# Kernel tuning notes

Measured on AMD Instinct MI355X. Metric: run time of the kernel, lower is better.

The kernel has to match this reference:

```python
import jax, jax.numpy as jnp
import numpy as np

B, S, SE, D, V, L, H = 32, 256, 1024, 512, 8000, 4, 8
EPS = 1e-3   # keras BatchNormalization default epsilon
NEG = -1e9


def _heads(x, W, b):
    Bx, Sx, Dx = x.shape
    return (jnp.einsum('bsd,de->bse', x, W) + b).reshape(Bx, Sx, H, Dx // H).transpose(0, 2, 1, 3)


def mha(q_in, kv_in, Wq, bq, Wk, bk, Wv, bv, Wo, bo, causal):
    dk = q_in.shape[-1] // H
    q = _heads(q_in, Wq, bq)   # [B,H,Sq,dk]
    k = _heads(kv_in, Wk, bk)  # [B,H,Sk,dk]
    v = _heads(kv_in, Wv, bv)
    scores = jnp.einsum('bhqd,bhkd->bhqk', q, k) / jnp.sqrt(jnp.asarray(dk, q.dtype))
    if causal:
        # original loop uses values = x[:, :j, :] -> token j attends to STRICTLY previous tokens;
        # token 0 has zero keys, so its attention output is exactly zero (before Wo bias).
        Sq, Sk = scores.shape[-2], scores.shape[-1]
        mask = jnp.arange(Sk)[None, :] < jnp.arange(Sq)[:, None]
        attn = jax.nn.softmax(jnp.where(mask, scores, NEG), axis=-1)
        attn = jnp.where(mask, attn, 0.0)
    else:
        attn = jax.nn.softmax(scores, axis=-1)
    out = jnp.einsum('bhqk,bhkd->bhqd', attn, v)
    out = out.transpose(0, 2, 1, 3).reshape(q_in.shape[0], q_in.shape[1], -1)
    return out @ Wo + bo


def bn(x, gamma, beta, mean, var):
    # keras BatchNorm, inference mode, axis=-1
    return gamma * (x - mean) * jax.lax.rsqrt(var + EPS) + beta


def setup_inputs():
    key = jax.random.key(0)
    ks = iter(jax.random.split(key, 80))

    def rn(*shape):
        return jax.random.normal(next(ks), shape, jnp.float32) * 0.02

    inp = {
        'sequence': jax.random.randint(next(ks), (B, S), 0, V, jnp.int32),
        'encoder_output': jax.random.normal(next(ks), (B, SE, D), jnp.float32),
        'pos_encodings': jax.random.normal(next(ks), (S, D), jnp.float32),
        'emb': rn(V, D),
        'Wout': rn(D, V), 'bout': jnp.zeros((V,), jnp.float32),
        'W1': rn(L, D, 512), 'b1': jnp.zeros((L, 512), jnp.float32),
        'W2': rn(L, 512, D), 'b2': jnp.zeros((L, D), jnp.float32),
    }
    for p in ('bot', 'mid'):
        for nm in ('Wq', 'Wk', 'Wv', 'Wo'):
            inp[f'{nm}_{p}'] = rn(L, D, D)
        for nm in ('bq', 'bk', 'bv', 'bo'):
            inp[f'{nm}_{p}'] = jnp.zeros((L, D), jnp.float32)
    for p in ('bot', 'mid', 'ffn'):
        inp[f'gamma_{p}'] = jnp.ones((L, D), jnp.float32)
        inp[f'beta_{p}'] = jnp.zeros((L, D), jnp.float32)
        inp[f'mean_{p}'] = jnp.zeros((L, D), jnp.float32)
        inp[f'var_{p}'] = jnp.ones((L, D), jnp.float32)
    return inp


def reference(sequence, encoder_output, pos_encodings, emb, Wout, bout, W1, b1, W2, b2,
              Wq_bot, Wk_bot, Wv_bot, Wo_bot, bq_bot, bk_bot, bv_bot, bo_bot,
              Wq_mid, Wk_mid, Wv_mid, Wo_mid, bq_mid, bk_mid, bv_mid, bo_mid,
              gamma_bot, beta_bot, mean_bot, var_bot,
              gamma_mid, beta_mid, mean_mid, var_mid,
              gamma_ffn, beta_ffn, mean_ffn, var_ffn):
    x = emb[sequence] + pos_encodings[None, :, :]  # [B,S,D]
    for i in range(L):
        a = mha(x, x, Wq_bot[i], bq_bot[i], Wk_bot[i], bk_bot[i], Wv_bot[i], bv_bot[i], Wo_bot[i], bo_bot[i], True)
        x = bn(x + a, gamma_bot[i], beta_bot[i], mean_bot[i], var_bot[i])
        a = mha(x, encoder_output, Wq_mid[i], bq_mid[i], Wk_mid[i], bk_mid[i], Wv_mid[i], bv_mid[i], Wo_mid[i], bo_mid[i], False)
        x = bn(x + a, gamma_mid[i], beta_mid[i], mean_mid[i], var_mid[i])
        f = jax.nn.relu(x @ W1[i] + b1[i]) @ W2[i] + b2[i]
        x = bn(x + f, gamma_ffn[i], beta_ffn[i], mean_ffn[i], var_ffn[i])
    return x @ Wout + bout  # logits [B,S,V]
```

## Files before the change

### kernel.cpp

```cpp
#include <hip/hip_runtime.h>
#include <hip/hip_fp16.h>

typedef _Float16 half8 __attribute__((ext_vector_type(8)));
typedef _Float16 half4 __attribute__((ext_vector_type(4)));
typedef float floatx4 __attribute__((ext_vector_type(4)));

#define NB 32
#define NS 256
#define NSE 1024
#define ND 512
#define NV 8000
#define NVP 8064
#define NL 4
#define NH 8
#define NDK 64
#define BN_EPS 1e-3f

typedef const __attribute__((address_space(1))) void* gas_ptr;
typedef __attribute__((address_space(3))) void* las_ptr;
__device__ __forceinline__ void gload16(const void* g, void* l) {
    __builtin_amdgcn_global_load_lds((gas_ptr)g, (las_ptr)l, 16, 0, 0);
}

__global__ __launch_bounds__(256) void k_cast(const float* __restrict__ in, _Float16* __restrict__ out) {
    size_t i = ((size_t)blockIdx.x * 256 + threadIdx.x) * 8;
    float4 a = *(const float4*)(in + i);
    float4 b = *(const float4*)(in + i + 4);
    half8 o;
    o[0] = (_Float16)a.x; o[1] = (_Float16)a.y; o[2] = (_Float16)a.z; o[3] = (_Float16)a.w;
    o[4] = (_Float16)b.x; o[5] = (_Float16)b.y; o[6] = (_Float16)b.z; o[7] = (_Float16)b.w;
    *(half8*)(out + i) = o;
}

__global__ __launch_bounds__(256) void k_embed(const int* __restrict__ seq,
                                               const float* __restrict__ emb,
                                               const float* __restrict__ pos,
                                               _Float16* __restrict__ x) {
    size_t i = ((size_t)blockIdx.x * 256 + threadIdx.x) * 8;
    int tok = (int)(i / ND);
    int d = (int)(i % ND);
    int s = tok % NS;
    int t = seq[tok];
    const float* ep = emb + (size_t)t * ND + d;
    const float* pp = pos + (size_t)s * ND + d;
    half8 o;
    for (int j = 0; j < 8; j++) o[j] = (_Float16)(ep[j] + pp[j]);
    *(half8*)(x + i) = o;
}

__global__ void k_transpose_w(const float* __restrict__ in, _Float16* __restrict__ out, int R, int C,
                              long long ostride) {
    __shared__ float tile[32][33];
    int b = blockIdx.z;
    int c0 = blockIdx.x * 32, r0 = blockIdx.y * 32;
    const float* pin = in + (size_t)b * R * C;
    _Float16* pout = out + (size_t)b * ostride;
    int tx = threadIdx.x, ty = threadIdx.y;
    for (int j = 0; j < 32; j += 8)
        tile[ty + j][tx] = pin[(size_t)(r0 + ty + j) * C + c0 + tx];
    __syncthreads();
    for (int j = 0; j < 32; j += 8)
        pout[(size_t)(c0 + ty + j) * R + r0 + tx] = (_Float16)tile[tx][ty + j];
}

template<int BM, int BK>
__global__ __launch_bounds__(256) void k_gemm(
    const _Float16* __restrict__ A, const _Float16* __restrict__ Bt,
    const float* __restrict__ bias0, const float* __restrict__ bias1, const float* __restrict__ bias2,
    void* __restrict__ C0, void* __restrict__ C1, void* __restrict__ C2,
    int M, int N, int K, int relu, int mode, int Sb,
    const _Float16* __restrict__ xres,
    const float* __restrict__ bng, const float* __restrict__ bnb,
    const float* __restrict__ bnm, const float* __restrict__ bnv) {
    constexpr int BN = 128;
    constexpr int MI = BM / 32;
    constexpr int TPR = BK / 8;
    constexpr int RPW = 64 / TPR;
    constexpr int RPI = 4 * RPW;
    __shared__ __align__(16) _Float16 smem[(BM + BN) * BK];
    _Float16* As = smem;
    _Float16* Bs = smem + BM * BK;

    int tid = threadIdx.x;
    int wid = tid >> 6, lane = tid & 63, quad = lane >> 4, r = lane & 15;

    int nwg = gridDim.x * gridDim.y;
    int orig = blockIdx.y * gridDim.x + blockIdx.x;
    int q8 = nwg >> 3, r8 = nwg & 7;
    int xcd = orig & 7, loc = orig >> 3;
    int swz = (xcd < r8 ? xcd * (q8 + 1) : r8 * (q8 + 1) + (xcd - r8) * q8) + loc;
    int m0 = (swz / gridDim.x) * BM;
    int n0 = (swz % gridDim.x) * BN;

    int wm = (wid >> 1) * (BM / 2);
    int wn = (wid & 1) * 64;

    floatx4 zf = {0.f, 0.f, 0.f, 0.f};
    floatx4 acc[MI][4];
    for (int i = 0; i < MI; i++) for (int j = 0; j < 4; j++) acc[i][j] = zf;

    int srow = wid * RPW + lane / TPR;
    int scol = (lane % TPR) * 8;

    for (int k0 = 0; k0 < K; k0 += BK) {
        __syncthreads();
        {
            const _Float16* abase = A + (size_t)(m0 + srow) * K + k0 + scol;
            _Float16* asl = As + (size_t)(wid * RPW) * BK;
#pragma unroll
            for (int i = 0; i < BM / RPI; i++)
                gload16(abase + (size_t)(i * RPI) * K, asl + (size_t)(i * RPI) * BK);
            const _Float16* bbase = Bt + (size_t)(n0 + srow) * K + k0 + scol;
            _Float16* bsl = Bs + (size_t)(wid * RPW) * BK;
#pragma unroll
            for (int i = 0; i < BN / RPI; i++)
                gload16(bbase + (size_t)(i * RPI) * K, bsl + (size_t)(i * RPI) * BK);
        }
        __syncthreads();
#pragma unroll
        for (int ks = 0; ks < BK; ks += 32) {
            half8 af[MI], bg[4];
#pragma unroll
            for (int i = 0; i < MI; i++) af[i] = *(const half8*)&As[(wm + i * 16 + r) * BK + ks + quad * 8];
#pragma unroll
            for (int j = 0; j < 4; j++)  bg[j] = *(const half8*)&Bs[(wn + j * 16 + r) * BK + ks + quad * 8];
#pragma unroll
            for (int i = 0; i < MI; i++)
#pragma unroll
                for (int j = 0; j < 4; j++)
                    acc[i][j] = __builtin_amdgcn_mfma_f32_16x16x32_f16(af[i], bg[j], acc[i][j], 0, 0, 0);
        }
    }

    __syncthreads();

    int seg = 0, nloc = n0, om = mode;
    const float* bias = bias0;
    char* C = (char*)C0;
    if (mode == 4) {
        seg = n0 >> 9; nloc = n0 & 511;
        om = (seg == 2) ? 1 : 0;
        C = (char*)(seg == 0 ? C0 : (seg == 1 ? C1 : C2));
        bias = (seg == 0) ? bias0 : ((seg == 1) ? bias1 : bias2);
    } else if (mode == 5) {
        seg = n0 >> 9; nloc = n0 & 511;
        om = seg ? 1 : 0;
        C = (char*)(seg ? C1 : C0);
        bias = seg ? bias1 : bias0;
    }

    if (om == 1) {
        for (int i = 0; i < MI; i++) {
            int grow = m0 + wm + i * 16 + quad * 4;
            int b = grow / Sb, s = grow - b * Sb;
            _Float16* outp = (_Float16*)C + (size_t)b * 512 * Sb + s;
#pragma unroll
            for (int j = 0; j < 4; j++) {
                int cb = nloc + wn + j * 16 + r;
                float bv = bias[cb];
                half4 h;
#pragma unroll
                for (int g = 0; g < 4; g++) h[g] = (_Float16)(acc[i][j][g] + bv);
                *(half4*)(outp + (size_t)cb * Sb) = h;
            }
        }
    } else {
        float* Ep = (float*)(void*)smem + wid * (16 * 68);
        int rr = lane >> 4;
        int c = (lane & 15) * 4;
        for (int i = 0; i < MI; i++) {
#pragma unroll
            for (int j = 0; j < 4; j++) {
                int cb = nloc + wn + j * 16 + r;
                float bv = (om == 2) ? (cb < N ? bias[cb] : 0.0f) : bias[cb];
#pragma unroll
                for (int g = 0; g < 4; g++) {
                    float v = acc[i][j][g] + bv;
                    if (relu) v = fmaxf(v, 0.0f);
                    Ep[(quad * 4 + g) * 68 + j * 16 + r] = v;
                }
            }
            int grow0 = m0 + wm + i * 16;
            int cb = nloc + wn + c;
            if (om == 0) {
#pragma unroll
                for (int p = 0; p < 4; p++) {
                    float4 v = *(float4*)&Ep[(p * 4 + rr) * 68 + c];
                    half4 h;
                    h[0] = (_Float16)v.x; h[1] = (_Float16)v.y; h[2] = (_Float16)v.z; h[3] = (_Float16)v.w;
                    *(half4*)&((_Float16*)C)[(size_t)(grow0 + p * 4 + rr) * 512 + cb] = h;
                }
            } else if (om == 3) {
                float4 g4 = *(const float4*)(bng + cb);
                float4 b4 = *(const float4*)(bnb + cb);
                float4 m4 = *(const float4*)(bnm + cb);
                float4 v4 = *(const float4*)(bnv + cb);
                float s0 = g4.x * rsqrtf(v4.x + BN_EPS);
                float s1 = g4.y * rsqrtf(v4.y + BN_EPS);
                float s2 = g4.z * rsqrtf(v4.z + BN_EPS);
                float s3 = g4.w * rsqrtf(v4.w + BN_EPS);
#pragma unroll
                for (int p = 0; p < 4; p++) {
                    int grow = grow0 + p * 4 + rr;
                    float4 v = *(float4*)&Ep[(p * 4 + rr) * 68 + c];
                    half4 xv = *(const half4*)(xres + (size_t)grow * 512 + cb);
                    half4 h;
                    h[0] = (_Float16)((v.x + (float)xv[0] - m4.x) * s0 + b4.x);
                    h[1] = (_Float16)((v.y + (float)xv[1] - m4.y) * s1 + b4.y);
                    h[2] = (_Float16)((v.z + (float)xv[2] - m4.z) * s2 + b4.z);
                    h[3] = (_Float16)((v.w + (float)xv[3] - m4.w) * s3 + b4.w);
                    *(half4*)&((_Float16*)C)[(size_t)grow * 512 + cb] = h;
                }
            } else {
                if (cb < N) {
#pragma unroll
                    for (int p = 0; p < 4; p++) {
                        float4 v = *(float4*)&Ep[(p * 4 + rr) * 68 + c];
                        *(float4*)&((float*)C)[(size_t)(grow0 + p * 4 + rr) * N + cb] = v;
                    }
                }
            }
        }
    }
}

__global__ __launch_bounds__(256) void k_attn(const _Float16* __restrict__ Q, const _Float16* __restrict__ Kb,
                                              const _Float16* __restrict__ Vt, _Float16* __restrict__ O,
                                              int Sk, int causal) {
    __shared__ _Float16 Plds[4][16][72];
    int qt = blockIdx.x, h = blockIdx.y, b = blockIdx.z;
    int tid = threadIdx.x;
    int w = tid >> 6, lane = tid & 63, quad = lane >> 4, r = lane & 15;
    int qbase = qt * 64 + w * 16;

    floatx4 zf = {0.f, 0.f, 0.f, 0.f};
    half8 aq[2];
    const _Float16* qptr = Q + (size_t)(b * NS + qbase + r) * ND + h * NDK;
    aq[0] = *(const half8*)(qptr + quad * 8);
    aq[1] = *(const half8*)(qptr + 32 + quad * 8);

    floatx4 Of[4];
    for (int j = 0; j < 4; j++) Of[j] = zf;
    float mrow[4], lrow[4];
    for (int g = 0; g < 4; g++) { mrow[g] = -1e30f; lrow[g] = 0.0f; }

    int ntiles = causal ? (qt + 1) : (Sk >> 6);

    for (int kt = 0; kt < ntiles; kt++) {
        floatx4 sc[4];
        for (int j = 0; j < 4; j++) sc[j] = zf;
        for (int t = 0; t < 2; t++) {
            for (int j = 0; j < 4; j++) {
                const _Float16* kptr = Kb + (size_t)(b * Sk + kt * 64 + j * 16 + r) * ND + h * NDK + t * 32 + quad * 8;
                half8 bk = *(const half8*)kptr;
                sc[j] = __builtin_amdgcn_mfma_f32_16x16x32_f16(aq[t], bk, sc[j], 0, 0, 0);
            }
        }
        float s[4][4], tmax[4];
        for (int g = 0; g < 4; g++) tmax[g] = -1e30f;
        for (int j = 0; j < 4; j++) {
            int key = kt * 64 + j * 16 + r;
            for (int g = 0; g < 4; g++) {
                float v = sc[j][g] * 0.125f;
                int qi = qbase + quad * 4 + g;
                if (causal && key >= qi) v = -1e30f;
                s[j][g] = v;
                tmax[g] = fmaxf(tmax[g], v);
            }
        }
        for (int off = 1; off < 16; off <<= 1)
            for (int g = 0; g < 4; g++)
                tmax[g] = fmaxf(tmax[g], __shfl_xor(tmax[g], off, 64));
        float alpha[4], psum[4];
        for (int g = 0; g < 4; g++) {
            float mnew = fmaxf(mrow[g], tmax[g]);
            alpha[g] = (mnew <= -1e29f) ? 1.0f : __expf(mrow[g] - mnew);
            mrow[g] = mnew;
            psum[g] = 0.0f;
        }
        for (int j = 0; j < 4; j++) {
            for (int g = 0; g < 4; g++) {
                float p = (s[j][g] <= -1e29f) ? 0.0f : __expf(s[j][g] - mrow[g]);
                psum[g] += p;
                Plds[w][quad * 4 + g][j * 16 + r] = (_Float16)p;
            }
        }
        for (int off = 1; off < 16; off <<= 1)
            for (int g = 0; g < 4; g++)
                psum[g] += __shfl_xor(psum[g], off, 64);
        for (int g = 0; g < 4; g++) lrow[g] = lrow[g] * alpha[g] + psum[g];
        for (int j = 0; j < 4; j++)
            for (int g = 0; g < 4; g++)
                Of[j][g] *= alpha[g];
        __syncthreads();
        for (int t = 0; t < 2; t++) {
            half8 ap = *(const half8*)&Plds[w][r][t * 32 + quad * 8];
            for (int j = 0; j < 4; j++) {
                const _Float16* vptr = Vt + (size_t)((b * NH + h) * NDK + j * 16 + r) * Sk + kt * 64 + t * 32 + quad * 8;
                half8 bv = *(const half8*)vptr;
                Of[j] = __builtin_amdgcn_mfma_f32_16x16x32_f16(ap, bv, Of[j], 0, 0, 0);
            }
        }
        __syncthreads();
    }
    for (int j = 0; j < 4; j++) {
        for (int g = 0; g < 4; g++) {
            int row = qbase + quad * 4 + g;
            float inv = (lrow[g] > 0.f) ? 1.0f / lrow[g] : 0.0f;
            O[(size_t)(b * NS + row) * ND + h * NDK + j * 16 + r] = (_Float16)(Of[j][g] * inv);
        }
    }
}

extern "C" void kernel_launch(void* const* d_in, const int* in_sizes, int n_in,
                              void* d_out, int out_size, void* d_ws, size_t ws_size,
                              hipStream_t stream) {
    const int*   seq  = (const int*)d_in[0];
    const float* enc  = (const float*)d_in[1];
    const float* pos  = (const float*)d_in[2];
    const float* emb  = (const float*)d_in[3];
    const float* Wout = (const float*)d_in[4];
    const float* bout = (const float*)d_in[5];
    const float* W1   = (const float*)d_in[6];
    const float* b1   = (const float*)d_in[7];
    const float* W2   = (const float*)d_in[8];
    const float* b2   = (const float*)d_in[9];
    const float* Wq_bot = (const float*)d_in[10];
    const float* Wk_bot = (const float*)d_in[11];
    const float* Wv_bot = (const float*)d_in[12];
    const float* Wo_bot = (const float*)d_in[13];
    const float* bq_bot = (const float*)d_in[14];
    const float* bk_bot = (const float*)d_in[15];
    const float* bv_bot = (const float*)d_in[16];
    const float* bo_bot = (const float*)d_in[17];
    const float* Wq_mid = (const float*)d_in[18];
    const float* Wk_mid = (const float*)d_in[19];
    const float* Wv_mid = (const float*)d_in[20];
    const float* Wo_mid = (const float*)d_in[21];
    const float* bq_mid = (const float*)d_in[22];
    const float* bk_mid = (const float*)d_in[23];
    const float* bv_mid = (const float*)d_in[24];
    const float* bo_mid = (const float*)d_in[25];
    const float* gam[3] = {(const float*)d_in[26], (const float*)d_in[30], (const float*)d_in[34]};
    const float* bet[3] = {(const float*)d_in[27], (const float*)d_in[31], (const float*)d_in[35]};
    const float* mea[3] = {(const float*)d_in[28], (const float*)d_in[32], (const float*)d_in[36]};
    const float* vr [3] = {(const float*)d_in[29], (const float*)d_in[33], (const float*)d_in[37]};

    char* wp = (char*)d_ws;
    auto alloc = [&](size_t elems) -> _Float16* {
        _Float16* p = (_Float16*)wp;
        wp += ((elems * 2 + 255) / 256) * 256;
        return p;
    };
    const size_t DD = (size_t)ND * ND;
    _Float16* WqkvTb = alloc(NL * 3 * DD);
    _Float16* WoTb   = alloc(NL * DD);
    _Float16* WqTm   = alloc(NL * DD);
    _Float16* WkvTm  = alloc(NL * 2 * DD);
    _Float16* WoTm   = alloc(NL * DD);
    _Float16* W1T    = alloc(NL * DD);
    _Float16* W2T    = alloc(NL * DD);
    _Float16* WoutT  = alloc((size_t)NVP * ND);
    const size_t XSZ = (size_t)NB * NS * ND;
    _Float16* x   = alloc(XSZ);
    _Float16* qb  = alloc(XSZ);
    _Float16* kb  = alloc(XSZ);
    _Float16* vts = alloc(XSZ);
    _Float16* ao  = alloc(XSZ);
    const size_t ESZ = (size_t)NB * NSE * ND;
    _Float16* ench  = alloc(ESZ);
    _Float16* kenc  = alloc(ESZ);
    _Float16* vtenc = alloc(ESZ);

    hipMemsetAsync(WoutT + (size_t)NV * ND, 0, (size_t)(NVP - NV) * ND * sizeof(_Float16), stream);

    dim3 tb(32, 8);
    const long long S1 = (long long)DD, S2 = (long long)(2 * DD), S3 = (long long)(3 * DD);
    k_transpose_w<<<dim3(16, 16, NL), tb, 0, stream>>>(Wq_bot, WqkvTb,          ND, ND, S3);
    k_transpose_w<<<dim3(16, 16, NL), tb, 0, stream>>>(Wk_bot, WqkvTb + DD,     ND, ND, S3);
    k_transpose_w<<<dim3(16, 16, NL), tb, 0, stream>>>(Wv_bot, WqkvTb + 2 * DD, ND, ND, S3);
    k_transpose_w<<<dim3(16, 16, NL), tb, 0, stream>>>(Wo_bot, WoTb,            ND, ND, S1);
    k_transpose_w<<<dim3(16, 16, NL), tb, 0, stream>>>(Wq_mid, WqTm,            ND, ND, S1);
    k_transpose_w<<<dim3(16, 16, NL), tb, 0, stream>>>(Wk_mid, WkvTm,           ND, ND, S2);
    k_transpose_w<<<dim3(16, 16, NL), tb, 0, stream>>>(Wv_mid, WkvTm + DD,      ND, ND, S2);
    k_transpose_w<<<dim3(16, 16, NL), tb, 0, stream>>>(Wo_mid, WoTm,            ND, ND, S1);
    k_transpose_w<<<dim3(16, 16, NL), tb, 0, stream>>>(W1,     W1T,             ND, ND, S1);
    k_transpose_w<<<dim3(16, 16, NL), tb, 0, stream>>>(W2,     W2T,             ND, ND, S1);
    k_transpose_w<<<dim3(NV / 32, 16, 1), tb, 0, stream>>>(Wout, WoutT, ND, NV, S1);
    k_cast<<<dim3((int)(ESZ / 8 / 256)), 256, 0, stream>>>(enc, ench);
    k_embed<<<dim3((int)(XSZ / 8 / 256)), 256, 0, stream>>>(seq, emb, pos, x);

    auto gemm64 = [&](const _Float16* A, const _Float16* Bt, const float* b0, void* Cp,
                      int relu, int mode, const _Float16* xr, const float* g, const float* be,
                      const float* me, const float* ve) {
        k_gemm<64, 128><<<dim3(4, 128), 256, 0, stream>>>(A, Bt, b0, nullptr, nullptr,
            Cp, nullptr, nullptr, 8192, 512, 512, relu, mode, 0, xr, g, be, me, ve);
    };

    for (int l = 0; l < NL; l++) {
        size_t wofs = (size_t)l * DD;
        size_t bofs = (size_t)l * ND;
        k_gemm<128, 64><<<dim3(12, 64), 256, 0, stream>>>(x, WqkvTb + (size_t)l * 3 * DD,
            bq_bot + bofs, bk_bot + bofs, bv_bot + bofs, qb, kb, vts,
            8192, 1536, 512, 0, 4, NS, nullptr, nullptr, nullptr, nullptr, nullptr);
        k_attn<<<dim3(NS / 64, NH, NB), 256, 0, stream>>>(qb, kb, vts, ao, NS, 1);
        gemm64(ao, WoTb + wofs, bo_bot + bofs, x, 0, 3, x,
               gam[0] + bofs, bet[0] + bofs, mea[0] + bofs, vr[0] + bofs);
        gemm64(x, WqTm + wofs, bq_mid + bofs, qb, 0, 0, nullptr, nullptr, nullptr, nullptr, nullptr);
        k_gemm<128, 64><<<dim3(8, 256), 256, 0, stream>>>(ench, WkvTm + (size_t)l * 2 * DD,
            bk_mid + bofs, bv_mid + bofs, nullptr, kenc, vtenc, nullptr,
            32768, 1024, 512, 0, 5, NSE, nullptr, nullptr, nullptr, nullptr, nullptr);
        k_attn<<<dim3(NS / 64, NH, NB), 256, 0, stream>>>(qb, kenc, vtenc, ao, NSE, 0);
        gemm64(ao, WoTm + wofs, bo_mid + bofs, x, 0, 3, x,
               gam[1] + bofs, bet[1] + bofs, mea[1] + bofs, vr[1] + bofs);
        gemm64(x, W1T + wofs, b1 + bofs, qb, 1, 0, nullptr, nullptr, nullptr, nullptr, nullptr);
        gemm64(qb, W2T + wofs, b2 + bofs, x, 0, 3, x,
               gam[2] + bofs, bet[2] + bofs, mea[2] + bofs, vr[2] + bofs);
    }
    k_gemm<128, 64><<<dim3(63, 64), 256, 0, stream>>>(x, WoutT, bout, nullptr, nullptr,
        d_out, nullptr, nullptr, 8192, NV, 512, 0, 2, 0, nullptr, nullptr, nullptr, nullptr, nullptr);
}
```

Before: 1.972 ms.

## Double-buffer GEMM LDS tiles with XOR swizzle and fixed BK of 64

```diff
diff --git a/kernel.cpp b/kernel.cpp
--- a/kernel.cpp
+++ b/kernel.cpp
@@ -63,7 +63,7 @@
         pout[(size_t)(c0 + ty + j) * R + r0 + tx] = (_Float16)tile[tx][ty + j];
 }
 
-template<int BM, int BK>
+template<int BM>
 __global__ __launch_bounds__(256) void k_gemm(
     const _Float16* __restrict__ A, const _Float16* __restrict__ Bt,
     const float* __restrict__ bias0, const float* __restrict__ bias1, const float* __restrict__ bias2,
@@ -73,13 +73,11 @@
     const float* __restrict__ bng, const float* __restrict__ bnb,
     const float* __restrict__ bnm, const float* __restrict__ bnv) {
     constexpr int BN = 128;
+    constexpr int BK = 64;
     constexpr int MI = BM / 32;
-    constexpr int TPR = BK / 8;
-    constexpr int RPW = 64 / TPR;
-    constexpr int RPI = 4 * RPW;
-    __shared__ __align__(16) _Float16 smem[(BM + BN) * BK];
-    _Float16* As = smem;
-    _Float16* Bs = smem + BM * BK;
+    constexpr int BUFH = (BM + BN) * BK;
+    constexpr int LA = (BM + BN) / 32;
+    __shared__ __align__(16) _Float16 smem[2 * BUFH];
 
     int tid = threadIdx.x;
     int wid = tid >> 6, lane = tid & 63, quad = lane >> 4, r = lane & 15;
@@ -99,40 +97,57 @@
     floatx4 acc[MI][4];
     for (int i = 0; i < MI; i++) for (int j = 0; j < 4; j++) acc[i][j] = zf;
 
-    int srow = wid * RPW + lane / TPR;
-    int scol = (lane % TPR) * 8;
-
-    for (int k0 = 0; k0 < K; k0 += BK) {
-        __syncthreads();
-        {
-            const _Float16* abase = A + (size_t)(m0 + srow) * K + k0 + scol;
-            _Float16* asl = As + (size_t)(wid * RPW) * BK;
-#pragma unroll
-            for (int i = 0; i < BM / RPI; i++)
-                gload16(abase + (size_t)(i * RPI) * K, asl + (size_t)(i * RPI) * BK);
-            const _Float16* bbase = Bt + (size_t)(n0 + srow) * K + k0 + scol;
-            _Float16* bsl = Bs + (size_t)(wid * RPW) * BK;
-#pragma unroll
-            for (int i = 0; i < BN / RPI; i++)
-                gload16(bbase + (size_t)(i * RPI) * K, bsl + (size_t)(i * RPI) * BK);
-        }
-        __syncthreads();
+    int srow = wid * 8 + (lane >> 3);
+    int scol = (((lane & 7) ^ ((lane >> 3) & 7)) << 3);
+
+    auto stage = [&](int k0, int buf) {
+        _Float16* As = smem + buf * BUFH;
+        _Float16* Bs = As + BM * BK;
+        const _Float16* abase = A + (size_t)(m0 + srow) * K + k0 + scol;
+        _Float16* asl = As + (wid * 8) * BK;
+#pragma unroll
+        for (int i = 0; i < BM / 32; i++)
+            gload16(abase + (size_t)(i * 32) * K, asl + (i * 32) * BK);
+        const _Float16* bbase = Bt + (size_t)(n0 + srow) * K + k0 + scol;
+        _Float16* bsl = Bs + (wid * 8) * BK;
+#pragma unroll
+        for (int i = 0; i < 4; i++)
+            gload16(bbase + (size_t)(i * 32) * K, bsl + (i * 32) * BK);
+    };
+
+    int NT = K / BK;
+    int cur = 0;
+    stage(0, 0);
+    for (int t = 0; t < NT; t++) {
+        if (t + 1 < NT) {
+            stage((t + 1) * BK, cur ^ 1);
+            asm volatile("s_waitcnt vmcnt(%0)" :: "n"(LA) : "memory");
+        } else {
+            asm volatile("s_waitcnt vmcnt(0)" ::: "memory");
+        }
+        __builtin_amdgcn_s_barrier();
+        const _Float16* As = smem + cur * BUFH;
+        const _Float16* Bs = As + BM * BK;
 #pragma unroll
         for (int ks = 0; ks < BK; ks += 32) {
             half8 af[MI], bg[4];
 #pragma unroll
-            for (int i = 0; i < MI; i++) af[i] = *(const half8*)&As[(wm + i * 16 + r) * BK + ks + quad * 8];
-#pragma unroll
-            for (int j = 0; j < 4; j++)  bg[j] = *(const half8*)&Bs[(wn + j * 16 + r) * BK + ks + quad * 8];
+            for (int i = 0; i < MI; i++)
+                af[i] = *(const half8*)&As[(wm + i * 16 + r) * BK + ((((ks >> 3) + quad) ^ (r & 7)) << 3)];
+#pragma unroll
+            for (int j = 0; j < 4; j++)
+                bg[j] = *(const half8*)&Bs[(wn + j * 16 + r) * BK + ((((ks >> 3) + quad) ^ (r & 7)) << 3)];
 #pragma unroll
             for (int i = 0; i < MI; i++)
 #pragma unroll
                 for (int j = 0; j < 4; j++)
                     acc[i][j] = __builtin_amdgcn_mfma_f32_16x16x32_f16(af[i], bg[j], acc[i][j], 0, 0, 0);
         }
-    }
-
-    __syncthreads();
+        if (t + 1 < NT) {
+            __builtin_amdgcn_s_barrier();
+            cur ^= 1;
+        }
+    }
 
     int seg = 0, nloc = n0, om = mode;
     const float* bias = bias0;
@@ -165,7 +180,7 @@
             }
         }
     } else {
-        float* Ep = (float*)(void*)smem + wid * (16 * 68);
+        float* Ep = (float*)(void*)(smem + (cur ^ 1) * BUFH) + wid * (16 * 68);
         int rr = lane >> 4;
         int c = (lane & 15) * 4;
         for (int i = 0; i < MI; i++) {
@@ -393,21 +408,21 @@
     auto gemm64 = [&](const _Float16* A, const _Float16* Bt, const float* b0, void* Cp,
                       int relu, int mode, const _Float16* xr, const float* g, const float* be,
                       const float* me, const float* ve) {
-        k_gemm<64, 128><<<dim3(4, 128), 256, 0, stream>>>(A, Bt, b0, nullptr, nullptr,
+        k_gemm<64><<<dim3(4, 128), 256, 0, stream>>>(A, Bt, b0, nullptr, nullptr,
             Cp, nullptr, nullptr, 8192, 512, 512, relu, mode, 0, xr, g, be, me, ve);
     };
 
     for (int l = 0; l < NL; l++) {
         size_t wofs = (size_t)l * DD;
         size_t bofs = (size_t)l * ND;
-        k_gemm<128, 64><<<dim3(12, 64), 256, 0, stream>>>(x, WqkvTb + (size_t)l * 3 * DD,
+        k_gemm<128><<<dim3(12, 64), 256, 0, stream>>>(x, WqkvTb + (size_t)l * 3 * DD,
             bq_bot + bofs, bk_bot + bofs, bv_bot + bofs, qb, kb, vts,
             8192, 1536, 512, 0, 4, NS, nullptr, nullptr, nullptr, nullptr, nullptr);
         k_attn<<<dim3(NS / 64, NH, NB), 256, 0, stream>>>(qb, kb, vts, ao, NS, 1);
         gemm64(ao, WoTb + wofs, bo_bot + bofs, x, 0, 3, x,
                gam[0] + bofs, bet[0] + bofs, mea[0] + bofs, vr[0] + bofs);
         gemm64(x, WqTm + wofs, bq_mid + bofs, qb, 0, 0, nullptr, nullptr, nullptr, nullptr, nullptr);
-        k_gemm<128, 64><<<dim3(8, 256), 256, 0, stream>>>(ench, WkvTm + (size_t)l * 2 * DD,
+        k_gemm<128><<<dim3(8, 256), 256, 0, stream>>>(ench, WkvTm + (size_t)l * 2 * DD,
             bk_mid + bofs, bv_mid + bofs, nullptr, kenc, vtenc, nullptr,
             32768, 1024, 512, 0, 5, NSE, nullptr, nullptr, nullptr, nullptr, nullptr);
         k_attn<<<dim3(NS / 64, NH, NB), 256, 0, stream>>>(qb, kenc, vtenc, ao, NSE, 0);
@@ -417,6 +432,6 @@
         gemm64(qb, W2T + wofs, b2 + bofs, x, 0, 3, x,
                gam[2] + bofs, bet[2] + bofs, mea[2] + bofs, vr[2] + bofs);
     }
-    k_gemm<128, 64><<<dim3(63, 64), 256, 0, stream>>>(x, WoutT, bout, nullptr, nullptr,
+    k_gemm<128><<<dim3(63, 64), 256, 0, stream>>>(x, WoutT, bout, nullptr, nullptr,
         d_out, nullptr, nullptr, 8192, NV, 512, 0, 2, 0, nullptr, nullptr, nullptr, nullptr, nullptr);
 }
```

New measurement: 1.765 ms. -10.5%, faster.
